# Kernel tuning notes

Measured on AMD Instinct MI355X. Metric: run time of the kernel, lower is better.

The kernel has to match this reference:

```python
import jax, jax.numpy as jnp
import numpy as np

N, IN_DIM, HEADS, C = 50000, 78, 10, 78
HC = HEADS * C          # 780
E = 400000
B = 256
NEG_SLOPE = 0.2


def setup_inputs() -> dict:
    key = jax.random.key(0)
    ks = jax.random.split(key, 10)
    x = jax.random.normal(ks[0], (N, IN_DIM), dtype=jnp.float32)
    edge_index = jax.random.randint(ks[1], (2, E), 0, N, dtype=jnp.int64)
    batch = jnp.sort(jax.random.randint(ks[2], (N,), 0, B, dtype=jnp.int64))
    s = 1.0 / np.sqrt(IN_DIM)
    W_l = jax.random.uniform(ks[3], (IN_DIM, HC), jnp.float32, -s, s)
    W_r = jax.random.uniform(ks[4], (IN_DIM, HC), jnp.float32, -s, s)
    att = jax.random.uniform(ks[5], (HEADS, C), jnp.float32, -1.0 / np.sqrt(C), 1.0 / np.sqrt(C))
    bias1 = jnp.zeros((HC,), jnp.float32)
    s2 = 1.0 / np.sqrt(HC)
    W_gcn = jax.random.uniform(ks[6], (HC, HC), jnp.float32, -s2, s2)
    bias_gcn = jnp.zeros((HC,), jnp.float32)
    return {"x": x, "edge_index": edge_index, "batch": batch,
            "W_l": W_l, "W_r": W_r, "att": att, "bias1": bias1,
            "W_gcn": W_gcn, "bias_gcn": bias_gcn}


def _add_self_loops(edge_index, n):
    loops = jnp.arange(n, dtype=edge_index.dtype)
    return jnp.concatenate([edge_index, jnp.stack([loops, loops])], axis=1)


def _gatv2(x, edge_index, W_l, W_r, att, bias):
    ei = _add_self_loops(edge_index, x.shape[0])
    src, dst = ei[0], ei[1]                      # message j -> i
    xl = (x @ W_l).reshape(-1, HEADS, C)         # [N,H,C]
    xr = (x @ W_r).reshape(-1, HEADS, C)
    e = xl[src] + xr[dst]                        # [E',H,C]
    e = jnp.where(e > 0, e, NEG_SLOPE * e)       # leaky_relu
    score = jnp.einsum('ehc,hc->eh', e, att)     # [E',H]
    # segment softmax over destination node
    m = jax.ops.segment_max(score, dst, num_segments=x.shape[0])
    ex = jnp.exp(score - m[dst])
    denom = jax.ops.segment_sum(ex, dst, num_segments=x.shape[0])
    alpha = ex / denom[dst]                      # [E',H]
    out = jax.ops.segment_sum(alpha[:, :, None] * xl[src], dst,
                              num_segments=x.shape[0])  # [N,H,C]
    return out.reshape(-1, HC) + bias


def _gcn(x, edge_index, W, bias):
    n = x.shape[0]
    ei = _add_self_loops(edge_index, n)
    src, dst = ei[0], ei[1]
    deg = jax.ops.segment_sum(jnp.ones_like(src, dtype=x.dtype), dst, num_segments=n)
    dinv = jax.lax.rsqrt(jnp.maximum(deg, 1e-12))
    norm = dinv[src] * dinv[dst]                 # [E']
    h = x @ W
    out = jax.ops.segment_sum(norm[:, None] * h[src], dst, num_segments=n)
    return out + bias


def reference(x, edge_index, batch, W_l, W_r, att, bias1, W_gcn, bias_gcn):
    # eval mode: dropout = identity
    h = jax.nn.elu(_gatv2(x, edge_index, W_l, W_r, att, bias1))
    h = _gcn(h, edge_index, W_gcn, bias_gcn)
    h = jax.nn.relu(h)
    gmax = jax.ops.segment_max(h, batch, num_segments=B)
    gmax = jnp.where(jnp.isfinite(gmax), gmax, 0.0)
    cnt = jax.ops.segment_sum(jnp.ones((h.shape[0], 1), h.dtype), batch, num_segments=B)
    gmean = jax.ops.segment_sum(h, batch, num_segments=B) / jnp.maximum(cnt, 1.0)
    return jnp.concatenate([gmax, gmean], axis=1)   # [B, 2*HC]
```

## Files before the change

### kernel.cpp

```cpp
#include <hip/hip_runtime.h>
#include <hip/hip_bf16.h>
#include <math.h>

#define NNODES   50000
#define INDIM    78
#define NHEADS   10
#define CDIM     78
#define HCDIM    780
#define NEDGES   400000
#define NBATCH   256
#define ETOT     (NEDGES + NNODES)
#define NEG_SLOPE 0.2f

#define BM 128
#define BN 128
#define BK 64
#define KPAD 832
#define NPAD 896
#define LDT 68

#define KP1 128
#define NP1 1664

typedef __attribute__((ext_vector_type(8))) short bf16x8_t;
typedef __attribute__((ext_vector_type(4))) float f32x4_t;
typedef __attribute__((ext_vector_type(2))) float v2f;

__device__ __forceinline__ float bf2f(unsigned short u) {
    union { unsigned int i; float f; } v; v.i = ((unsigned int)u) << 16; return v.f;
}
__device__ __forceinline__ unsigned short f2bf(float f) {
    __hip_bfloat16 h = __float2bfloat16(f);
    return *reinterpret_cast<unsigned short*>(&h);
}
__device__ __forceinline__ v2f cvt2(unsigned int u) {
    union { unsigned int i; float f; } lo, hi;
    lo.i = u << 16;
    hi.i = u & 0xFFFF0000u;
    v2f r; r.x = lo.f; r.y = hi.f; return r;
}
__device__ __forceinline__ v2f vabs2(v2f t) {
    union { v2f f; unsigned long long u; } x; x.f = t;
    x.u &= 0x7FFFFFFF7FFFFFFFull; return x.f;
}
__device__ __forceinline__ float dpp_red8(float x) {
    int y;
    y = __builtin_amdgcn_update_dpp(0, __float_as_int(x), 0xB1, 0xF, 0xF, true);
    x += __int_as_float(y);
    y = __builtin_amdgcn_update_dpp(0, __float_as_int(x), 0x4E, 0xF, 0xF, true);
    x += __int_as_float(y);
    y = __builtin_amdgcn_update_dpp(0, __float_as_int(x), 0x141, 0xF, 0xF, true);
    x += __int_as_float(y);
    return x;
}

__device__ __forceinline__ void async_ld16(const unsigned short* g, unsigned short* l) {
    __builtin_amdgcn_global_load_lds(
        (const __attribute__((address_space(1))) void*)g,
        (__attribute__((address_space(3))) void*)l, 16, 0, 0);
}

__global__ void zero_kernel(float* __restrict__ outp, int nf, int* __restrict__ deg, int ni) {
    int i = blockIdx.x * blockDim.x + threadIdx.x;
    if (i < nf) outp[i] = 0.f;
    if (i < ni) deg[i] = 0;
}

__global__ void count_kernel(const int* __restrict__ ei, int* __restrict__ deg) {
    int e = blockIdx.x * blockDim.x + threadIdx.x;
    if (e >= ETOT) return;
    int d = (e < NEDGES) ? ei[NEDGES + e] : (e - NEDGES);
    atomicAdd(&deg[d], 1);
}

__global__ void scan1_kernel(const int* __restrict__ deg, int* __restrict__ rowp,
                             int* __restrict__ bsum) {
    __shared__ int s[256];
    int t = threadIdx.x, b = blockIdx.x;
    int i = b * 256 + t;
    int v = (i < NNODES) ? deg[i] : 0;
    s[t] = v;
    __syncthreads();
    #pragma unroll
    for (int off = 1; off < 256; off <<= 1) {
        int y = (t >= off) ? s[t - off] : 0;
        __syncthreads();
        s[t] += y;
        __syncthreads();
    }
    int incl = s[t];
    if (i < NNODES) rowp[i] = incl - v;
    if (t == 255) bsum[b] = incl;
}

__global__ void scan2_kernel(int* __restrict__ bsum, int* __restrict__ rowp, int nblk,
                             const int* __restrict__ batch, int* __restrict__ bst) {
    __shared__ int s[256];
    int t = threadIdx.x;
    int v = 0;
    if (t < 256) { v = (t < nblk) ? bsum[t] : 0; s[t] = v; }
    __syncthreads();
    #pragma unroll
    for (int off = 1; off < 256; off <<= 1) {
        int y = (t < 256 && t >= off) ? s[t - off] : 0;
        __syncthreads();
        if (t < 256) s[t] += y;
        __syncthreads();
    }
    if (t < 256) {
        int incl = s[t];
        if (t < nblk) bsum[t] = incl - v;
        if (t == 255) rowp[NNODES] = incl;
    } else {
        int b = t - 256;
        int lo = 0, hi = NNODES;
        while (lo < hi) { int mid = (lo + hi) >> 1; if (batch[mid] < b) lo = mid + 1; else hi = mid; }
        bst[b] = lo;
        if (t == 511) bst[NBATCH] = NNODES;
    }
}

__global__ void scan3_kernel(int* __restrict__ rowp, const int* __restrict__ bsum,
                             int* __restrict__ curs, const int* __restrict__ deg,
                             float* __restrict__ dinv) {
    int i = blockIdx.x * 256 + threadIdx.x;
    if (i >= NNODES) return;
    int r = rowp[i] + bsum[i >> 8];
    rowp[i] = r;
    curs[i] = r;
    dinv[i] = rsqrtf((float)deg[i]);
}

__global__ void fill_kernel(const int* __restrict__ ei,
                            int* __restrict__ cursor, int* __restrict__ col) {
    int e = blockIdx.x * blockDim.x + threadIdx.x;
    if (e >= ETOT) return;
    int s, d;
    if (e < NEDGES) { s = ei[e]; d = ei[NEDGES + e]; }
    else            { s = d = e - NEDGES; }
    int pos = atomicAdd(&cursor[d], 1);
    col[pos] = s;
}

__global__ void wprep_kernel(const float* __restrict__ Wl, const float* __restrict__ Wr,
                             unsigned short* __restrict__ Wc) {
    int idx = blockIdx.x * 256 + threadIdx.x;
    if (idx >= NP1 * KP1) return;
    int n = idx >> 7, k = idx & 127;
    float v = 0.f;
    if (k < INDIM) {
        if (n < HCDIM)            v = Wl[(size_t)k * HCDIM + n];
        else if (n < 2 * HCDIM)   v = Wr[(size_t)k * HCDIM + (n - HCDIM)];
    }
    Wc[idx] = f2bf(v);
}

__global__ __launch_bounds__(256) void gemm1_kernel(
        const float* __restrict__ x, const unsigned short* __restrict__ Wc,
        unsigned short* __restrict__ xl, unsigned short* __restrict__ xr, int M) {
    __shared__ unsigned short As[4 * 4096];
    __shared__ unsigned short Bs[4 * 4096];
    int t = threadIdx.x;
    int lane = t & 63, w = t >> 6;
    int bm = blockIdx.x * 128;

    for (int idx = t; idx < 128 * 128; idx += 256) {
        int row = idx >> 7, k = idx & 127;
        int kc = k >> 5, ch = (k >> 3) & 3, e = k & 7;
        int gr = bm + row;
        float v = (gr < M && k < INDIM) ? x[(size_t)gr * INDIM + k] : 0.f;
        As[kc * 4096 + row * 32 + (((ch + (row >> 1)) & 3) * 8) + e] = f2bf(v);
    }

    int lrow = lane >> 2;
    int gch = ((lane & 3) - (lane >> 3)) & 3;
    int m16 = lane & 15, q = lane >> 4;
    int wr = (w >> 1) * 64, wcc = (w & 1) * 64;

    for (int nb = 0; nb < 13; nb++) {
        __syncthreads();
        #pragma unroll
        for (int kc = 0; kc < 4; kc++) {
            const unsigned short* gb = Wc + ((size_t)(nb * 128 + 32 * w + lrow)) * KP1
                                          + kc * 32 + gch * 8;
            unsigned short* lb = Bs + kc * 4096 + (32 * w) * 32;
            async_ld16(gb, lb);
            async_ld16(gb + 16 * KP1, lb + 16 * 32);
        }
        __syncthreads();

        f32x4_t acc[4][4];
        #pragma unroll
        for (int i = 0; i < 4; i++)
            #pragma unroll
            for (int j = 0; j < 4; j++)
                acc[i][j] = (f32x4_t)(0.f);

        #pragma unroll
        for (int kc = 0; kc < 4; kc++) {
            bf16x8_t af[4], bf[4];
            #pragma unroll
            for (int i = 0; i < 4; i++) {
                int row = wr + i * 16 + m16;
                af[i] = *(const bf16x8_t*)&As[kc * 4096 + row * 32 + (((q + (row >> 1)) & 3) * 8)];
            }
            #pragma unroll
            for (int j = 0; j < 4; j++) {
                int row = wcc + j * 16 + m16;
                bf[j] = *(const bf16x8_t*)&Bs[kc * 4096 + row * 32 + (((q + (row >> 1)) & 3) * 8)];
            }
            #pragma unroll
            for (int i = 0; i < 4; i++)
                #pragma unroll
                for (int j = 0; j < 4; j++)
                    acc[i][j] = __builtin_amdgcn_mfma_f32_16x16x32_bf16(af[i], bf[j], acc[i][j], 0, 0, 0);
        }

        #pragma unroll
        for (int j = 0; j < 4; j++) {
            int ng = nb * 128 + wcc + j * 16 + m16;
            if (ng >= 2 * HCDIM) continue;
            unsigned short* dst = (ng < HCDIM) ? (xl + ng) : (xr + (ng - HCDIM));
            #pragma unroll
            for (int i = 0; i < 4; i++) {
                #pragma unroll
                for (int rr = 0; rr < 4; rr++) {
                    int row = bm + wr + i * 16 + q * 4 + rr;
                    if (row < M) dst[(size_t)row * HCDIM] = f2bf(acc[i][j][rr]);
                }
            }
        }
    }
}

__global__ __launch_bounds__(256) void gat_kernel(
        const unsigned short* __restrict__ xl, const unsigned short* xr,
        const int* __restrict__ row_ptr, const int* __restrict__ col,
        const float* __restrict__ att, const float* __restrict__ bias1,
        const float* __restrict__ dinv, unsigned short* h_out) {
    int wid = blockIdx.x * 4 + (threadIdx.x >> 6);
    int quad = wid / 5;
    int slot = wid - 5 * quad;
    if (quad >= NNODES / 4) return;
    int lane = threadIdx.x & 63;
    int g = lane >> 3, cl = lane & 7;
    bool lo7 = cl < 7;
    bool strad = (slot == 4);
    int node, head;
    if (!strad) { node = 4 * quad + slot;      head = g; }
    else        { node = 4 * quad + (g >> 1);  head = 8 + (g & 1); }
    int hcl = head * (CDIM / 2);
    const unsigned int* xlu = (const unsigned int*)xl;
    const unsigned int* xru = (const unsigned int*)xr;

    int off[5];
    off[0] = cl; off[1] = cl + 8; off[2] = cl + 16; off[3] = cl + 24;
    off[4] = lo7 ? cl + 32 : 38;

    const float L6 = 0.6f * 1.4426950408889634f;
    const float L4 = 0.4f * 1.4426950408889634f;
    const float2* ap = (const float2*)(att + head * CDIM);
    const unsigned int* xrp = xru + (size_t)node * (HCDIM / 2) + hcl;
    v2f a6[5], a4[5], r[5];
    #pragma unroll
    for (int k = 0; k < 5; k++) {
        float2 f = ap[off[k]];
        if (k == 4 && !lo7) { f.x = 0.f; f.y = 0.f; }
        a6[k].x = f.x * L6; a6[k].y = f.y * L6;
        a4[k].x = f.x * L4; a4[k].y = f.y * L4;
        r[k] = cvt2(xrp[off[k]]);
    }

    float l = 0.f;
    v2f acc[5];
    #pragma unroll
    for (int k = 0; k < 5; k++) acc[k] = (v2f)(0.f);

    if (!strad) {
        int e0 = row_ptr[node], e1 = row_ptr[node + 1];
        int e = e0;
        for (; e < e1; e++) {
            int j = __builtin_amdgcn_readfirstlane(col[e]);
            const unsigned int* xp = xlu + (size_t)j * (HCDIM / 2) + hcl;
            v2f v[5], s2 = (v2f)(0.f);
            #pragma unroll
            for (int k = 0; k < 5; k++) {
                v[k] = cvt2(xp[off[k]]);
                v2f t = v[k] + r[k];
                s2 += t * a6[k] + vabs2(t) * a4[k];
            }
            float p = __builtin_amdgcn_exp2f(dpp_red8(s2.x + s2.y));
            l += p;
            #pragma unroll
            for (int k = 0; k < 5; k++) acc[k] += p * v[k];
        }
    } else {
        int re0 = row_ptr[node], deg = row_ptr[node + 1] - re0;
        int d0 = __builtin_amdgcn_readlane(deg, 0);
        int d1 = __builtin_amdgcn_readlane(deg, 16);
        int d2 = __builtin_amdgcn_readlane(deg, 32);
        int d3 = __builtin_amdgcn_readlane(deg, 48);
        int iters = max(max(d0, d1), max(d2, d3));
        for (int i = 0; i < iters; i++) {
            bool live = i < deg;
            int ec = re0 + (live ? i : 0);
            int j = col[ec];
            const unsigned int* xp = xlu + (size_t)j * (HCDIM / 2) + hcl;
            v2f v[5], s2 = (v2f)(0.f);
            #pragma unroll
            for (int k = 0; k < 5; k++) {
                v[k] = cvt2(xp[off[k]]);
                v2f t = v[k] + r[k];
                s2 += t * a6[k] + vabs2(t) * a4[k];
            }
            float p = __builtin_amdgcn_exp2f(dpp_red8(s2.x + s2.y));
            p = live ? p : 0.f;
            l += p;
            #pragma unroll
            for (int k = 0; k < 5; k++) acc[k] += p * v[k];
        }
    }

    float inv = 1.f / l;
    float dn = dinv[node];
    size_t rbase = (size_t)node * HCDIM + head * CDIM;
    const float2* bp = (const float2*)(bias1 + head * CDIM);
    unsigned int* op = (unsigned int*)(h_out + rbase);
    #pragma unroll
    for (int k = 0; k < 5; k++) {
        if (k == 4 && !lo7) break;
        float2 bb = bp[off[k]];
        float x0 = acc[k].x * inv + bb.x;
        float x1 = acc[k].y * inv + bb.y;
        x0 = x0 > 0.f ? x0 : (__expf(x0) - 1.f);
        x1 = x1 > 0.f ? x1 : (__expf(x1) - 1.f);
        x0 *= dn; x1 *= dn;
        unsigned int o = (unsigned int)f2bf(x0) | ((unsigned int)f2bf(x1) << 16);
        op[off[k]] = o;
    }
}

__global__ __launch_bounds__(256) void gcn_agg_kernel(
        const unsigned short* __restrict__ h, const int* __restrict__ row_ptr,
        const int* __restrict__ col, const float* __restrict__ dinv,
        unsigned short* __restrict__ agg) {
    int node = blockIdx.x * 4 + (threadIdx.x >> 6);
    if (node >= NNODES) return;
    int ln = threadIdx.x & 63;
    bool hasC = ln < 3;
    float accA[8] = {}, accB[4] = {}, accC[4] = {};
    int e0 = row_ptr[node], e1 = row_ptr[node + 1];
    int e = e0;
    int jn = (e < e1) ? col[e] : 0;
    for (; e < e1; ) {
        int j = __builtin_amdgcn_readfirstlane(jn);
        ++e;
        jn = (e < e1) ? col[e] : 0;
        const unsigned short* hr = h + (size_t)j * HCDIM;
        bf16x8_t u = *(const bf16x8_t*)(hr + 8 * ln);
        ushort4 v4 = *(const ushort4*)(hr + 512 + 4 * ln);
        ushort4 w4 = hasC ? *(const ushort4*)(hr + 768 + 4 * ln) : make_ushort4(0, 0, 0, 0);
        #pragma unroll
        for (int k = 0; k < 8; k++) accA[k] += bf2f((unsigned short)u[k]);
        accB[0] += bf2f(v4.x);
        accB[1] += bf2f(v4.y);
        accB[2] += bf2f(v4.z);
        accB[3] += bf2f(v4.w);
        accC[0] += bf2f(w4.x);
        accC[1] += bf2f(w4.y);
        accC[2] += bf2f(w4.z);
        accC[3] += bf2f(w4.w);
    }
    float di = dinv[node];
    unsigned short* ar = agg + (size_t)node * HCDIM;
    ushort4 o1, o2, ob;
    o1.x = f2bf(accA[0] * di); o1.y = f2bf(accA[1] * di);
    o1.z = f2bf(accA[2] * di); o1.w = f2bf(accA[3] * di);
    o2.x = f2bf(accA[4] * di); o2.y = f2bf(accA[5] * di);
    o2.z = f2bf(accA[6] * di); o2.w = f2bf(accA[7] * di);
    ob.x = f2bf(accB[0] * di); ob.y = f2bf(accB[1] * di);
    ob.z = f2bf(accB[2] * di); ob.w = f2bf(accB[3] * di);
    *(ushort4*)(ar + 8 * ln) = o1;
    *(ushort4*)(ar + 8 * ln + 4) = o2;
    *(ushort4*)(ar + 512 + 4 * ln) = ob;
    if (hasC) {
        ushort4 oc;
        oc.x = f2bf(accC[0] * di); oc.y = f2bf(accC[1] * di);
        oc.z = f2bf(accC[2] * di); oc.w = f2bf(accC[3] * di);
        *(ushort4*)(ar + 768 + 4 * ln) = oc;
    }
}

__global__ void btprep_kernel(const float* __restrict__ W, unsigned short* __restrict__ BT) {
    int idx = blockIdx.x * 256 + threadIdx.x;
    if (idx >= NPAD * KPAD) return;
    int n = idx / KPAD, k = idx - n * KPAD;
    float v = (n < HCDIM && k < HCDIM) ? W[(size_t)k * HCDIM + n] : 0.f;
    BT[idx] = f2bf(v);
}

__global__ __launch_bounds__(256) void gemm2_pool_kernel(
        const unsigned short* __restrict__ A, const unsigned short* __restrict__ BT,
        const float* __restrict__ bias, const int* __restrict__ batch,
        float* __restrict__ out, int M) {
    int f = blockIdx.x;
    int xcd = f & 7, inner = f >> 3;
    int bq = inner / 7, colt = inner - 7 * bq;
    int band = 8 * bq + xcd;
    if (band >= (M + BM - 1) / BM) return;
    int bm = band * BM, bn = colt * BN;

    __shared__ unsigned short smem[2 * 128 * 64];
    unsigned short* As = smem;
    unsigned short* Bs = smem + 128 * 64;
    __shared__ int bsh[BM];

    int t = threadIdx.x;
    int lane = t & 63, w = t >> 6;

    if (t < BM) {
        int row = bm + t;
        bsh[t] = (row < M) ? batch[row] : -1;
    }

    int m16 = lane & 15, q = lane >> 4;
    int wr = (w >> 1) * 64, wc = (w & 1) * 64;

    int lrow8 = lane >> 3;
    int c8 = lane & 7;
    int gch = (c8 - lrow8) & 7;
    const unsigned short* gA = A  + (size_t)(bm + 32 * w + lrow8) * HCDIM + gch * 8;
    const unsigned short* gB = BT + (size_t)(bn + 32 * w + lrow8) * KPAD  + gch * 8;
    unsigned short* lA = As + (32 * w) * 64;
    unsigned short* lB = Bs + (32 * w) * 64;

    f32x4_t acc[4][4];
    #pragma unroll
    for (int i = 0; i < 4; i++)
        #pragma unroll
        for (int j = 0; j < 4; j++)
            acc[i][j] = (f32x4_t)(0.f);

    for (int k0 = 0; k0 < KPAD; k0 += BK) {
        __syncthreads();
        #pragma unroll
        for (int ib = 0; ib < 4; ib++) {
            async_ld16(gA + (size_t)(8 * ib) * HCDIM + k0, lA + (8 * ib) * 64);
            async_ld16(gB + (size_t)(8 * ib) * KPAD  + k0, lB + (8 * ib) * 64);
        }
        __syncthreads();

        #pragma unroll
        for (int half = 0; half < 2; half++) {
            bf16x8_t af[4], bf[4];
            #pragma unroll
            for (int i = 0; i < 4; i++) {
                int row = wr + i * 16 + m16;
                af[i] = *(const bf16x8_t*)&As[row * 64 + ((4 * half + q + row) & 7) * 8];
            }
            #pragma unroll
            for (int j = 0; j < 4; j++) {
                int row = wc + j * 16 + m16;
                bf[j] = *(const bf16x8_t*)&Bs[row * 64 + ((4 * half + q + row) & 7) * 8];
            }
            #pragma unroll
            for (int i = 0; i < 4; i++)
                #pragma unroll
                for (int j = 0; j < 4; j++)
                    acc[i][j] = __builtin_amdgcn_mfma_f32_16x16x32_bf16(af[i], bf[j], acc[i][j], 0, 0, 0);
        }
    }

    float bvj[4];
    #pragma unroll
    for (int j = 0; j < 4; j++) {
        int gcc = bn + wc + j * 16 + m16;
        bvj[j] = (gcc < HCDIM) ? bias[gcc] : 0.f;
    }

    #pragma unroll
    for (int p = 0; p < 2; p++) {
        __syncthreads();
        if ((w >> 1) == p) {
            #pragma unroll
            for (int i = 0; i < 4; i++) {
                #pragma unroll
                for (int j = 0; j < 4; j++) {
                    int colc = wc + j * 16 + m16;
                    ushort4 o;
                    float v0 = acc[i][j][0] + bvj[j];
                    float v1 = acc[i][j][1] + bvj[j];
                    float v2 = acc[i][j][2] + bvj[j];
                    float v3 = acc[i][j][3] + bvj[j];
                    o.x = f2bf(v0 > 0.f ? v0 : 0.f);
                    o.y = f2bf(v1 > 0.f ? v1 : 0.f);
                    o.z = f2bf(v2 > 0.f ? v2 : 0.f);
                    o.w = f2bf(v3 > 0.f ? v3 : 0.f);
                    *(ushort4*)&smem[colc * LDT + i * 16 + q * 4] = o;
                }
            }
        }
        __syncthreads();
        int colp = t & 127;
        int rb = (t >> 7) * 32;
        int gc = bn + colp;
        if (gc < HCDIM) {
            int cur = -1; float mx = 0.f, sm = 0.f;
            bool done = false;
            for (int rr = rb; rr < rb + 32 && !done; rr += 4) {
                ushort4 u = *(const ushort4*)&smem[colp * LDT + rr];
                unsigned short us[4] = {u.x, u.y, u.z, u.w};
                #pragma unroll
                for (int s2 = 0; s2 < 4; s2++) {
                    int b = bsh[64 * p + rr + s2];
                    if (b < 0) { done = true; break; }
                    float v = bf2f(us[s2]);
                    if (b != cur) {
                        if (cur >= 0) {
                            atomicMax((int*)(out + (size_t)cur * (2 * HCDIM) + gc), __float_as_int(mx));
                            atomicAdd(out + (size_t)cur * (2 * HCDIM) + HCDIM + gc, sm);
                        }
                        cur = b; mx = v; sm = v;
                    } else { mx = fmaxf(mx, v); sm += v; }
                }
            }
            if (cur >= 0) {
                atomicMax((int*)(out + (size_t)cur * (2 * HCDIM) + gc), __float_as_int(mx));
                atomicAdd(out + (size_t)cur * (2 * HCDIM) + HCDIM + gc, sm);
            }
        }
    }
}

__global__ void finalize_kernel(float* __restrict__ out, const int* __restrict__ bst) {
    int i = blockIdx.x * blockDim.x + threadIdx.x;
    if (i >= NBATCH * HCDIM) return;
    int b = i / HCDIM, c = i - b * HCDIM;
    int cnt = bst[b + 1] - bst[b];
    out[(size_t)b * (2 * HCDIM) + HCDIM + c] /= (float)(cnt > 0 ? cnt : 1);
}

extern "C" void kernel_launch(void* const* d_in, const int* in_sizes, int n_in,
                              void* d_out, int out_size, void* d_ws, size_t ws_size,
                              hipStream_t stream) {
    const float* x       = (const float*)d_in[0];
    const int*   ei      = (const int*)d_in[1];
    const int*   batch   = (const int*)d_in[2];
    const float* W_l     = (const float*)d_in[3];
    const float* W_r     = (const float*)d_in[4];
    const float* att     = (const float*)d_in[5];
    const float* bias1   = (const float*)d_in[6];
    const float* W_gcn   = (const float*)d_in[7];
    const float* bias_gcn= (const float*)d_in[8];
    float* out = (float*)d_out;

    char* w = (char*)d_ws;
    const size_t BIGH = (size_t)NNODES * HCDIM * sizeof(unsigned short);
    unsigned short* xl  = (unsigned short*)(w);
    unsigned short* xr  = (unsigned short*)(w + BIGH);
    unsigned short* agg = xl;
    unsigned short* BT  = xr;
    char* sm = w + 2 * BIGH;
    int*   rowp = (int*)(sm);                    sm += 50048 * 4;
    int*   col  = (int*)(sm);                    sm += 450048 * 4;
    float* dinv = (float*)(sm);                  sm += 50048 * 4;
    int*   bst  = (int*)(sm);                    sm += 512 * 4;
    int*   bsum = (int*)(sm);                    sm += 256 * 4;
    char* S = sm;                                sm += 426240;
    int*   deg  = (int*)(S);
    int*   curs = (int*)(S + 200192);
    unsigned short* Wc = (unsigned short*)(S);
    size_t needed = (size_t)(sm - (char*)d_ws);
    if (ws_size < needed) return;

    zero_kernel<<<(NBATCH * 2 * HCDIM + 255) / 256, 256, 0, stream>>>(
        out, NBATCH * 2 * HCDIM, deg, NNODES);

    {
        int eblocks = (ETOT + 255) / 256;
        int nblocks = (NNODES + 255) / 256;
        count_kernel<<<eblocks, 256, 0, stream>>>(ei, deg);
        scan1_kernel<<<nblocks, 256, 0, stream>>>(deg, rowp, bsum);
        scan2_kernel<<<1, 512, 0, stream>>>(bsum, rowp, nblocks, batch, bst);
        scan3_kernel<<<nblocks, 256, 0, stream>>>(rowp, bsum, curs, deg, dinv);
        fill_kernel<<<eblocks, 256, 0, stream>>>(ei, curs, col);
    }

    wprep_kernel<<<(NP1 * KP1 + 255) / 256, 256, 0, stream>>>(W_l, W_r, Wc);

    gemm1_kernel<<<(NNODES + 127) / 128, 256, 0, stream>>>(x, Wc, xl, xr, NNODES);

    {
        int waves = (NNODES / 4) * 5;
        int blocks = waves / 4;
        gat_kernel<<<blocks, 256, 0, stream>>>(xl, xr, rowp, col, att, bias1, dinv, xr);
    }

    gcn_agg_kernel<<<(NNODES + 3) / 4, 256, 0, stream>>>(xr, rowp, col, dinv, agg);

    btprep_kernel<<<(NPAD * KPAD + 255) / 256, 256, 0, stream>>>(W_gcn, BT);

    {
        int nb = (NNODES + BM - 1) / BM;
        int gx = 8 * ((nb + 7) / 8) * 7;
        gemm2_pool_kernel<<<gx, 256, 0, stream>>>(agg, BT, bias_gcn, batch, out, NNODES);
    }

    finalize_kernel<<<(NBATCH * HCDIM + 255) / 256, 256, 0, stream>>>(out, bst);
}
```

Measured before the change: 647.5 us.

## Double-buffer LDS tiles in gemm2_pool with BK 32 prefetch

Restructures the K loop of the second GEMM (fused with pooling) into a two-stage LDS double buffer. Each stage is a 32-wide K slice, and the next slice's async global-to-LDS loads are issued before the MFMAs on the current slice. This removes one barrier per iteration and aims to hide global load latency behind matrix math. In exchange, K iterations double and the swizzle shrinks to 4 chunks, which could raise LDS bank conflicts or loop overhead.

```diff
diff --git a/kernel.cpp b/kernel.cpp
--- a/kernel.cpp
+++ b/kernel.cpp
@@ -14,7 +14,7 @@
 
 #define BM 128
 #define BN 128
-#define BK 64
+#define BK2 32
 #define KPAD 832
 #define NPAD 896
 #define LDT 68
@@ -410,9 +410,7 @@
     if (band >= (M + BM - 1) / BM) return;
     int bm = band * BM, bn = colt * BN;
 
-    __shared__ unsigned short smem[2 * 128 * 64];
-    unsigned short* As = smem;
-    unsigned short* Bs = smem + 128 * 64;
+    __shared__ unsigned short smem[16384];
     __shared__ int bsh[BM];
 
     int t = threadIdx.x;
@@ -426,13 +424,17 @@
     int m16 = lane & 15, q = lane >> 4;
     int wr = (w >> 1) * 64, wc = (w & 1) * 64;
 
-    int lrow8 = lane >> 3;
-    int c8 = lane & 7;
-    int gch = (c8 - lrow8) & 7;
-    const unsigned short* gA = A  + (size_t)(bm + 32 * w + lrow8) * HCDIM + gch * 8;
-    const unsigned short* gB = BT + (size_t)(bn + 32 * w + lrow8) * KPAD  + gch * 8;
-    unsigned short* lA = As + (32 * w) * 64;
-    unsigned short* lB = Bs + (32 * w) * 64;
+    int lrow = lane >> 2;
+    int c4 = lane & 3;
+    int gch = (c4 - (lrow & 3)) & 3;
+    const unsigned short* gA = A  + (size_t)(bm + 32 * w + lrow) * HCDIM + gch * 8;
+    const unsigned short* gB = BT + (size_t)(bn + 32 * w + lrow) * KPAD  + gch * 8;
+    int lbase = (32 * w) * 32;
+
+    async_ld16(gA, smem + lbase);
+    async_ld16(gA + 16 * HCDIM, smem + lbase + 512);
+    async_ld16(gB, smem + 4096 + lbase);
+    async_ld16(gB + 16 * KPAD, smem + 4096 + lbase + 512);
 
     f32x4_t acc[4][4];
     #pragma unroll
@@ -441,34 +443,35 @@
         for (int j = 0; j < 4; j++)
             acc[i][j] = (f32x4_t)(0.f);
 
-    for (int k0 = 0; k0 < KPAD; k0 += BK) {
-        __syncthreads();
-        #pragma unroll
-        for (int ib = 0; ib < 4; ib++) {
-            async_ld16(gA + (size_t)(8 * ib) * HCDIM + k0, lA + (8 * ib) * 64);
-            async_ld16(gB + (size_t)(8 * ib) * KPAD  + k0, lB + (8 * ib) * 64);
-        }
-        __syncthreads();
-
-        #pragma unroll
-        for (int half = 0; half < 2; half++) {
-            bf16x8_t af[4], bf[4];
-            #pragma unroll
-            for (int i = 0; i < 4; i++) {
-                int row = wr + i * 16 + m16;
-                af[i] = *(const bf16x8_t*)&As[row * 64 + ((4 * half + q + row) & 7) * 8];
-            }
-            #pragma unroll
-            for (int j = 0; j < 4; j++) {
-                int row = wc + j * 16 + m16;
-                bf[j] = *(const bf16x8_t*)&Bs[row * 64 + ((4 * half + q + row) & 7) * 8];
-            }
-            #pragma unroll
-            for (int i = 0; i < 4; i++)
-                #pragma unroll
-                for (int j = 0; j < 4; j++)
-                    acc[i][j] = __builtin_amdgcn_mfma_f32_16x16x32_bf16(af[i], bf[j], acc[i][j], 0, 0, 0);
-        }
+    int kb = 0;
+    for (int k0 = 0; k0 < KPAD; k0 += BK2, kb ^= 1) {
+        __syncthreads();
+        if (k0 + BK2 < KPAD) {
+            unsigned short* nb = smem + (kb ^ 1) * 8192;
+            int kn = k0 + BK2;
+            async_ld16(gA + kn, nb + lbase);
+            async_ld16(gA + 16 * HCDIM + kn, nb + lbase + 512);
+            async_ld16(gB + kn, nb + 4096 + lbase);
+            async_ld16(gB + 16 * KPAD + kn, nb + 4096 + lbase + 512);
+        }
+        const unsigned short* As = smem + kb * 8192;
+        const unsigned short* Bs = As + 4096;
+        bf16x8_t af[4], bf[4];
+        #pragma unroll
+        for (int i = 0; i < 4; i++) {
+            int row = wr + i * 16 + m16;
+            af[i] = *(const bf16x8_t*)&As[row * 32 + ((q + row) & 3) * 8];
+        }
+        #pragma unroll
+        for (int j = 0; j < 4; j++) {
+            int row = wc + j * 16 + m16;
+            bf[j] = *(const bf16x8_t*)&Bs[row * 32 + ((q + row) & 3) * 8];
+        }
+        #pragma unroll
+        for (int i = 0; i < 4; i++)
+            #pragma unroll
+            for (int j = 0; j < 4; j++)
+                acc[i][j] = __builtin_amdgcn_mfma_f32_16x16x32_bf16(af[i], bf[j], acc[i][j], 0, 0, 0);
     }
 
     float bvj[4];
```

Result: slower. 664.3 us (+2.6%).

## Load GEMM2 MFMA operands directly from global memory with register double-buffering

Applied to the files above, without the earlier changes.

The second GEMM (fused with pooling) no longer stages A and B tiles through LDS with async loads and barriers. Each wave now loads its own bf16x8 fragments straight from global memory into registers, prefetching the next k-half while the current one feeds MFMAs. This removes the per-iteration __syncthreads and the LDS round trip. In exchange, each fragment is fetched by two waves, relying on the caches to absorb the duplicate reads, and global-load latency is hidden by only a two-stage register pipeline. The final prefetch also reads past the padded K range.

```diff
diff --git a/kernel.cpp b/kernel.cpp
--- a/kernel.cpp
+++ b/kernel.cpp
@@ -14,7 +14,6 @@
 
 #define BM 128
 #define BN 128
-#define BK 64
 #define KPAD 832
 #define NPAD 896
 #define LDT 68
@@ -410,9 +409,7 @@
     if (band >= (M + BM - 1) / BM) return;
     int bm = band * BM, bn = colt * BN;
 
-    __shared__ unsigned short smem[2 * 128 * 64];
-    unsigned short* As = smem;
-    unsigned short* Bs = smem + 128 * 64;
+    __shared__ unsigned short smem[128 * LDT];
     __shared__ int bsh[BM];
 
     int t = threadIdx.x;
@@ -426,13 +423,13 @@
     int m16 = lane & 15, q = lane >> 4;
     int wr = (w >> 1) * 64, wc = (w & 1) * 64;
 
-    int lrow8 = lane >> 3;
-    int c8 = lane & 7;
-    int gch = (c8 - lrow8) & 7;
-    const unsigned short* gA = A  + (size_t)(bm + 32 * w + lrow8) * HCDIM + gch * 8;
-    const unsigned short* gB = BT + (size_t)(bn + 32 * w + lrow8) * KPAD  + gch * 8;
-    unsigned short* lA = As + (32 * w) * 64;
-    unsigned short* lB = Bs + (32 * w) * 64;
+    const unsigned short* pa[4];
+    const unsigned short* pb[4];
+    #pragma unroll
+    for (int i = 0; i < 4; i++) {
+        pa[i] = A  + (size_t)(bm + wr + i * 16 + m16) * HCDIM + q * 8;
+        pb[i] = BT + (size_t)(bn + wc + i * 16 + m16) * KPAD  + q * 8;
+    }
 
     f32x4_t acc[4][4];
     #pragma unroll
@@ -441,34 +438,33 @@
         for (int j = 0; j < 4; j++)
             acc[i][j] = (f32x4_t)(0.f);
 
-    for (int k0 = 0; k0 < KPAD; k0 += BK) {
-        __syncthreads();
-        #pragma unroll
-        for (int ib = 0; ib < 4; ib++) {
-            async_ld16(gA + (size_t)(8 * ib) * HCDIM + k0, lA + (8 * ib) * 64);
-            async_ld16(gB + (size_t)(8 * ib) * KPAD  + k0, lB + (8 * ib) * 64);
-        }
-        __syncthreads();
-
-        #pragma unroll
-        for (int half = 0; half < 2; half++) {
-            bf16x8_t af[4], bf[4];
-            #pragma unroll
-            for (int i = 0; i < 4; i++) {
-                int row = wr + i * 16 + m16;
-                af[i] = *(const bf16x8_t*)&As[row * 64 + ((4 * half + q + row) & 7) * 8];
-            }
-            #pragma unroll
-            for (int j = 0; j < 4; j++) {
-                int row = wc + j * 16 + m16;
-                bf[j] = *(const bf16x8_t*)&Bs[row * 64 + ((4 * half + q + row) & 7) * 8];
-            }
-            #pragma unroll
-            for (int i = 0; i < 4; i++)
-                #pragma unroll
-                for (int j = 0; j < 4; j++)
-                    acc[i][j] = __builtin_amdgcn_mfma_f32_16x16x32_bf16(af[i], bf[j], acc[i][j], 0, 0, 0);
-        }
+    bf16x8_t af0[4], bf0[4], af1[4], bf1[4];
+    #pragma unroll
+    for (int i = 0; i < 4; i++) {
+        af0[i] = *(const bf16x8_t*)(pa[i]);
+        bf0[i] = *(const bf16x8_t*)(pb[i]);
+    }
+    for (int k0 = 0; k0 < KPAD; k0 += 64) {
+        #pragma unroll
+        for (int i = 0; i < 4; i++) {
+            af1[i] = *(const bf16x8_t*)(pa[i] + k0 + 32);
+            bf1[i] = *(const bf16x8_t*)(pb[i] + k0 + 32);
+        }
+        #pragma unroll
+        for (int i = 0; i < 4; i++)
+            #pragma unroll
+            for (int j = 0; j < 4; j++)
+                acc[i][j] = __builtin_amdgcn_mfma_f32_16x16x32_bf16(af0[i], bf0[j], acc[i][j], 0, 0, 0);
+        #pragma unroll
+        for (int i = 0; i < 4; i++) {
+            af0[i] = *(const bf16x8_t*)(pa[i] + k0 + 64);
+            bf0[i] = *(const bf16x8_t*)(pb[i] + k0 + 64);
+        }
+        #pragma unroll
+        for (int i = 0; i < 4; i++)
+            #pragma unroll
+            for (int j = 0; j < 4; j++)
+                acc[i][j] = __builtin_amdgcn_mfma_f32_16x16x32_bf16(af1[i], bf1[j], acc[i][j], 0, 0, 0);
     }
 
     float bvj[4];
```

Measured after the change: 746.7 us. +15.3%, slower.
